# Kernel optimization log

Hardware: AMD Instinct MI355X
Metric: run time of the kernel (lower is better)

The kernel has to match this reference:

```python
import jax, jax.numpy as jnp
import numpy as np

SEQ, BS, D, F, E = 1024, 2, 2048, 2048, 8


def setup_inputs() -> dict:
    key = jax.random.key(0)
    ks = jax.random.split(key, 8)
    s = 0.02  # param init scale
    return {
        "hidden_states": jax.random.normal(ks[0], (SEQ, BS, D), jnp.float32),
        "router_w": jax.random.normal(ks[1], (D, E), jnp.float32) * s,
        "gate_w": jax.random.normal(ks[2], (E, D, F), jnp.float32) * s,
        "up_w": jax.random.normal(ks[3], (E, D, F), jnp.float32) * s,
        "down_w": jax.random.normal(ks[4], (E, F, D), jnp.float32) * s,
        "shared_gate_w": jax.random.normal(ks[5], (D, F), jnp.float32) * s,
        "shared_up_w": jax.random.normal(ks[6], (D, F), jnp.float32) * s,
        "shared_down_w": jax.random.normal(ks[7], (F, D), jnp.float32) * s,
    }


def reference(hidden_states, router_w, gate_w, up_w, down_w,
              shared_gate_w, shared_up_w, shared_down_w):
    S, B, Dm = hidden_states.shape
    x = hidden_states.reshape(-1, Dm)          # [T, D] flattened tokens
    # --- router: top-1 expert, sigmoid gate applied to the selected logit ---
    logits = x @ router_w                      # [T, E]
    expert_idx = jnp.argmax(logits, axis=-1)   # top-1 index, [T]
    score = jax.nn.sigmoid(jnp.max(logits, axis=-1))  # [T]
    xs = x * score[:, None]                    # scale BEFORE expert (Llama4)
    # --- per-expert SwiGLU MLP on masked token sets, scatter-combined ---
    n_experts = router_w.shape[1]
    out = jnp.zeros_like(x)
    for e in range(n_experts):                 # small structural loop over experts
        m = (expert_idx == e)[:, None]
        xe = jnp.where(m, xs, 0.0)             # zeroed dispatch (equiv to gather)
        h = jax.nn.silu(xe @ gate_w[e]) * (xe @ up_w[e])
        out = out + jnp.where(m, h @ down_w[e], 0.0)
    # --- shared expert on all tokens ---
    shared = (jax.nn.silu(x @ shared_gate_w) * (x @ shared_up_w)) @ shared_down_w
    return (out + shared).reshape(S, B, Dm)
```

## Files before the change

### kernel.cpp

```cpp
#include <hip/hip_runtime.h>
#include <stdint.h>
#include <math.h>

#define T_TOK 2048
#define DIM   2048
#define FDIM  2048
#define NE    8

#define BM 128
#define BN 128
#define BK 32
#define LDB 40

typedef unsigned short u16;
typedef short s16x8 __attribute__((ext_vector_type(8)));
typedef float f32x4 __attribute__((ext_vector_type(4)));

__device__ __forceinline__ u16 f2bf(float f) {
    union { float f; unsigned int u; } v; v.f = f;
    unsigned int r = v.u + 0x7FFFu + ((v.u >> 16) & 1u);
    return (u16)(r >> 16);
}

__global__ __launch_bounds__(256) void router_k(
    const float* __restrict__ x, const float* __restrict__ rw,
    float* __restrict__ score, int* __restrict__ eidx, int* __restrict__ counts)
{
    int t = blockIdx.x;
    int tid = threadIdx.x;
    float p[8] = {0.f,0.f,0.f,0.f,0.f,0.f,0.f,0.f};
    const float* xrow = x + (size_t)t * DIM;
    for (int d = tid; d < DIM; d += 256) {
        float xv = xrow[d];
        const float4* r = (const float4*)(rw + (size_t)d * 8);
        float4 r0 = r[0], r1 = r[1];
        p[0] += xv * r0.x; p[1] += xv * r0.y; p[2] += xv * r0.z; p[3] += xv * r0.w;
        p[4] += xv * r1.x; p[5] += xv * r1.y; p[6] += xv * r1.z; p[7] += xv * r1.w;
    }
    #pragma unroll
    for (int off = 32; off > 0; off >>= 1) {
        #pragma unroll
        for (int e = 0; e < 8; ++e) p[e] += __shfl_down(p[e], off);
    }
    __shared__ float red[4][8];
    int wave = tid >> 6, lane = tid & 63;
    if (lane == 0) {
        #pragma unroll
        for (int e = 0; e < 8; ++e) red[wave][e] = p[e];
    }
    __syncthreads();
    if (tid == 0) {
        float lg[8];
        #pragma unroll
        for (int e = 0; e < 8; ++e) lg[e] = red[0][e] + red[1][e] + red[2][e] + red[3][e];
        int best = 0; float bv = lg[0];
        #pragma unroll
        for (int e = 1; e < 8; ++e) { if (lg[e] > bv) { bv = lg[e]; best = e; } }
        score[t] = 1.f / (1.f + expf(-bv));
        eidx[t] = best;
        atomicAdd(&counts[best], 1);
    }
}

__global__ void scan_k(const int* __restrict__ counts, int* __restrict__ offs,
                       int* __restrict__ fill)
{
    if (threadIdx.x == 0 && blockIdx.x == 0) {
        int run = 0;
        for (int e = 0; e < NE; ++e) { offs[e] = run; fill[e] = run; run += counts[e]; }
    }
}

__global__ __launch_bounds__(256) void gather_k(
    const float* __restrict__ x, const float* __restrict__ score,
    const int* __restrict__ eidx, int* __restrict__ fill,
    int* __restrict__ tokmap, u16* __restrict__ xsc, u16* __restrict__ xbf)
{
    int t = blockIdx.x, tid = threadIdx.x;
    __shared__ int sp;
    if (tid == 0) {
        int e = eidx[t];
        int p = atomicAdd(&fill[e], 1);
        tokmap[p] = t;
        sp = p;
    }
    __syncthreads();
    int pos = sp;
    float s = score[t];
    const float4* xr = (const float4*)(x + (size_t)t * DIM);
    float4 a = xr[tid * 2], b = xr[tid * 2 + 1];
    alignas(16) u16 raw[8] = { f2bf(a.x), f2bf(a.y), f2bf(a.z), f2bf(a.w),
                               f2bf(b.x), f2bf(b.y), f2bf(b.z), f2bf(b.w) };
    alignas(16) u16 scl[8] = { f2bf(a.x*s), f2bf(a.y*s), f2bf(a.z*s), f2bf(a.w*s),
                               f2bf(b.x*s), f2bf(b.y*s), f2bf(b.z*s), f2bf(b.w*s) };
    *(s16x8*)(xbf + (size_t)t * DIM + tid * 8)   = *(s16x8*)raw;
    *(s16x8*)(xsc + (size_t)pos * DIM + tid * 8) = *(s16x8*)scl;
}

__device__ __forceinline__ void stageB(const float* __restrict__ W, u16* Bs,
                                       int bn, int bkh)
{
    const float* wp = W + (size_t)bkh * FDIM + bn;
    alignas(16) u16 tmp[16];
    #pragma unroll
    for (int j = 0; j < 16; ++j) tmp[j] = f2bf(wp[(size_t)j * FDIM]);
    *(s16x8*)&Bs[bn * LDB + bkh]     = *(s16x8*)&tmp[0];
    *(s16x8*)&Bs[bn * LDB + bkh + 8] = *(s16x8*)&tmp[8];
}

__global__ __launch_bounds__(256) void gateup_k(
    const u16* __restrict__ xsc, const u16* __restrict__ xbf,
    const float* __restrict__ gate_w, const float* __restrict__ up_w,
    const float* __restrict__ sgw, const float* __restrict__ suw,
    const int* __restrict__ counts, const int* __restrict__ offs,
    u16* __restrict__ Hbf, u16* __restrict__ Hs)
{
    int bid = blockIdx.x;
    int g  = bid >> 8;
    int mt = (bid >> 4) & 15;
    int nt = bid & 15;

    int M; const u16* A; const float* Wg; const float* Wu; u16* Ho;
    if (g < NE) {
        M = counts[g];
        int ro = offs[g];
        A  = xsc + (size_t)ro * DIM;
        Wg = gate_w + (size_t)g * DIM * FDIM;
        Wu = up_w  + (size_t)g * DIM * FDIM;
        Ho = Hbf + (size_t)ro * FDIM;
    } else {
        M = T_TOK; A = xbf; Wg = sgw; Wu = suw; Ho = Hs;
    }
    int m0 = mt * BM;
    if (m0 >= M) return;
    int n0 = nt * BN;

    __shared__ u16 As[BM * BK];
    __shared__ u16 Bg[BN * LDB];
    __shared__ u16 Bu[BN * LDB];

    int tid  = threadIdx.x;
    int lane = tid & 63;
    int wave = tid >> 6;
    int wm = (wave >> 1) * 64;
    int wn = (wave & 1) * 64;

    f32x4 accg[4][4], accu[4][4];
    #pragma unroll
    for (int i = 0; i < 4; ++i)
        #pragma unroll
        for (int j = 0; j < 4; ++j) { accg[i][j] = (f32x4)0.f; accu[i][j] = (f32x4)0.f; }

    int ar = tid >> 2;
    int ac = (tid & 3) * 8;
    int arow0 = min(m0 + ar,      M - 1);
    int arow1 = min(m0 + 64 + ar, M - 1);

    int bn  = tid & 127;
    int bkh = (tid >> 7) * 16;

    int am   = wm + (lane & 15);
    int koff = (lane >> 4) * 8;

    for (int k0 = 0; k0 < DIM; k0 += BK) {
        *(s16x8*)&As[ar * BK + ac]        = *(const s16x8*)&A[(size_t)arow0 * DIM + k0 + ac];
        *(s16x8*)&As[(64 + ar) * BK + ac] = *(const s16x8*)&A[(size_t)arow1 * DIM + k0 + ac];
        stageB(Wg + (size_t)k0 * FDIM + n0, Bg, bn, bkh);
        stageB(Wu + (size_t)k0 * FDIM + n0, Bu, bn, bkh);
        __syncthreads();

        s16x8 af[4];
        #pragma unroll
        for (int i = 0; i < 4; ++i)
            af[i] = *(const s16x8*)&As[(am + i * 16) * BK + koff];
        #pragma unroll
        for (int j = 0; j < 4; ++j) {
            int bc = wn + j * 16 + (lane & 15);
            s16x8 bg = *(const s16x8*)&Bg[bc * LDB + koff];
            s16x8 bu = *(const s16x8*)&Bu[bc * LDB + koff];
            #pragma unroll
            for (int i = 0; i < 4; ++i) {
                accg[i][j] = __builtin_amdgcn_mfma_f32_16x16x32_bf16(af[i], bg, accg[i][j], 0, 0, 0);
                accu[i][j] = __builtin_amdgcn_mfma_f32_16x16x32_bf16(af[i], bu, accu[i][j], 0, 0, 0);
            }
        }
        __syncthreads();
    }

    int rbase = wm + ((lane >> 4) << 2);
    int cbase = n0 + wn + (lane & 15);
    #pragma unroll
    for (int i = 0; i < 4; ++i) {
        #pragma unroll
        for (int j = 0; j < 4; ++j) {
            #pragma unroll
            for (int r = 0; r < 4; ++r) {
                int row = m0 + rbase + i * 16 + r;
                if (row < M) {
                    float gv = accg[i][j][r];
                    float uv = accu[i][j][r];
                    float h = gv / (1.f + expf(-gv)) * uv;
                    Ho[(size_t)row * FDIM + cbase + j * 16] = f2bf(h);
                }
            }
        }
    }
}

__global__ __launch_bounds__(256) void down_k(
    const u16* __restrict__ Hbf, const u16* __restrict__ Hs,
    const float* __restrict__ down_w, const float* __restrict__ sdw,
    const int* __restrict__ counts, const int* __restrict__ offs,
    const int* __restrict__ tokmap, float* __restrict__ out)
{
    int bid = blockIdx.x;
    int g  = bid >> 8;
    int mt = (bid >> 4) & 15;
    int nt = bid & 15;

    int M, ro; const u16* A; const float* W;
    if (g < NE) {
        M = counts[g];
        ro = offs[g];
        A = Hbf + (size_t)ro * FDIM;
        W = down_w + (size_t)g * FDIM * DIM;
    } else {
        M = T_TOK; ro = 0; A = Hs; W = sdw;
    }
    int m0 = mt * BM;
    if (m0 >= M) return;
    int n0 = nt * BN;

    __shared__ u16 As[BM * BK];
    __shared__ u16 Bd[BN * LDB];

    int tid  = threadIdx.x;
    int lane = tid & 63;
    int wave = tid >> 6;
    int wm = (wave >> 1) * 64;
    int wn = (wave & 1) * 64;

    f32x4 acc[4][4];
    #pragma unroll
    for (int i = 0; i < 4; ++i)
        #pragma unroll
        for (int j = 0; j < 4; ++j) acc[i][j] = (f32x4)0.f;

    int ar = tid >> 2;
    int ac = (tid & 3) * 8;
    int arow0 = min(m0 + ar,      M - 1);
    int arow1 = min(m0 + 64 + ar, M - 1);
    int bn  = tid & 127;
    int bkh = (tid >> 7) * 16;

    int am   = wm + (lane & 15);
    int koff = (lane >> 4) * 8;

    for (int k0 = 0; k0 < FDIM; k0 += BK) {
        *(s16x8*)&As[ar * BK + ac]        = *(const s16x8*)&A[(size_t)arow0 * FDIM + k0 + ac];
        *(s16x8*)&As[(64 + ar) * BK + ac] = *(const s16x8*)&A[(size_t)arow1 * FDIM + k0 + ac];
        stageB(W + (size_t)k0 * DIM + n0, Bd, bn, bkh);
        __syncthreads();

        s16x8 af[4];
        #pragma unroll
        for (int i = 0; i < 4; ++i)
            af[i] = *(const s16x8*)&As[(am + i * 16) * BK + koff];
        #pragma unroll
        for (int j = 0; j < 4; ++j) {
            int bc = wn + j * 16 + (lane & 15);
            s16x8 bd = *(const s16x8*)&Bd[bc * LDB + koff];
            #pragma unroll
            for (int i = 0; i < 4; ++i)
                acc[i][j] = __builtin_amdgcn_mfma_f32_16x16x32_bf16(af[i], bd, acc[i][j], 0, 0, 0);
        }
        __syncthreads();
    }

    int rbase = wm + ((lane >> 4) << 2);
    int cbase = n0 + wn + (lane & 15);
    #pragma unroll
    for (int i = 0; i < 4; ++i) {
        #pragma unroll
        for (int r = 0; r < 4; ++r) {
            int row = m0 + rbase + i * 16 + r;
            if (row < M) {
                int tok = (g < NE) ? tokmap[ro + row] : row;
                #pragma unroll
                for (int j = 0; j < 4; ++j)
                    atomicAdd(&out[(size_t)tok * DIM + cbase + j * 16], acc[i][j][r]);
            }
        }
    }
}

extern "C" void kernel_launch(void* const* d_in, const int* in_sizes, int n_in,
                              void* d_out, int out_size, void* d_ws, size_t ws_size,
                              hipStream_t stream) {
    const float* x   = (const float*)d_in[0];
    const float* rw  = (const float*)d_in[1];
    const float* gw  = (const float*)d_in[2];
    const float* uw  = (const float*)d_in[3];
    const float* dw  = (const float*)d_in[4];
    const float* sgw = (const float*)d_in[5];
    const float* suw = (const float*)d_in[6];
    const float* sdw = (const float*)d_in[7];
    float* out = (float*)d_out;

    char* ws = (char*)d_ws;
    float* score = (float*)(ws);
    int* eidx    = (int*)(ws + 8192);
    int* counts  = (int*)(ws + 16384);
    int* fill    = (int*)(ws + 16448);
    int* offs    = (int*)(ws + 16512);
    int* tokmap  = (int*)(ws + 16576);
    u16* xsc = (u16*)(ws + 32768);
    u16* xbf = (u16*)(ws + 32768 + 1ull * 8388608);
    u16* Hbf = (u16*)(ws + 32768 + 2ull * 8388608);
    u16* Hs  = (u16*)(ws + 32768 + 3ull * 8388608);

    hipMemsetAsync(counts, 0, 128, stream);
    hipMemsetAsync(out, 0, (size_t)out_size * sizeof(float), stream);

    router_k<<<T_TOK, 256, 0, stream>>>(x, rw, score, eidx, counts);
    scan_k<<<1, 64, 0, stream>>>(counts, offs, fill);
    gather_k<<<T_TOK, 256, 0, stream>>>(x, score, eidx, fill, tokmap, xsc, xbf);
    gateup_k<<<NE * 256 + 256, 256, 0, stream>>>(xsc, xbf, gw, uw, sgw, suw,
                                                 counts, offs, Hbf, Hs);
    down_k<<<NE * 256 + 256, 256, 0, stream>>>(Hbf, Hs, dw, sdw,
                                               counts, offs, tokmap, out);
}
```

Measured before the change: 792.1 us.

## Pre-transpose weights to bf16 and use direct global-to-LDS loads in GEMMs

Adds a kernel that converts every fp32 weight matrix to bf16 once and transposes it to an N-major layout. The GEMM kernels can then load B tiles with global_load_lds 16-byte transfers instead of strided per-element fp32 loads converted in registers. M tile shrinks to 64, giving more blocks for small expert groups. The shared-expert down pass now writes output directly, which removes the output memset and the atomics; the expert pass then does plain read-add-write, relying on each token hitting one expert. The cost is an extra full pass over all weights (read fp32, write bf16) on every call, plus extra workspace.

```diff
diff --git a/kernel.cpp b/kernel.cpp
--- a/kernel.cpp
+++ b/kernel.cpp
@@ -7,10 +7,10 @@
 #define FDIM  2048
 #define NE    8
 
-#define BM 128
+#define BM 64
 #define BN 128
 #define BK 32
-#define LDB 40
+#define MATSZ 4194304ull
 
 typedef unsigned short u16;
 typedef short s16x8 __attribute__((ext_vector_type(8)));
@@ -20,6 +20,11 @@
     union { float f; unsigned int u; } v; v.f = f;
     unsigned int r = v.u + 0x7FFFu + ((v.u >> 16) & 1u);
     return (u16)(r >> 16);
+}
+
+__device__ __forceinline__ void gload_lds16(const void* g, void* l) {
+    __builtin_amdgcn_global_load_lds((const __attribute__((address_space(1))) void*)g,
+                                     (__attribute__((address_space(3))) void*)l, 16, 0, 0);
 }
 
 __global__ __launch_bounds__(256) void router_k(
@@ -97,100 +102,142 @@
     *(s16x8*)(xsc + (size_t)pos * DIM + tid * 8) = *(s16x8*)scl;
 }
 
-__device__ __forceinline__ void stageB(const float* __restrict__ W, u16* Bs,
-                                       int bn, int bkh)
-{
-    const float* wp = W + (size_t)bkh * FDIM + bn;
-    alignas(16) u16 tmp[16];
-    #pragma unroll
-    for (int j = 0; j < 16; ++j) tmp[j] = f2bf(wp[(size_t)j * FDIM]);
-    *(s16x8*)&Bs[bn * LDB + bkh]     = *(s16x8*)&tmp[0];
-    *(s16x8*)&Bs[bn * LDB + bkh + 8] = *(s16x8*)&tmp[8];
+#define TLDS 260
+__global__ __launch_bounds__(256) void wtrans_k(
+    const float* __restrict__ gw, const float* __restrict__ uw,
+    const float* __restrict__ dwn, const float* __restrict__ sgw,
+    const float* __restrict__ suw, const float* __restrict__ sdw,
+    u16* __restrict__ wt, int mstart)
+{
+    int bid = blockIdx.x;
+    int m = mstart + (bid >> 8);
+    int kt = (bid >> 3) & 31;
+    int nt = bid & 7;
+    const float* src;
+    if      (m < 8)   src = gw  + (size_t)m * MATSZ;
+    else if (m < 16)  src = uw  + (size_t)(m - 8) * MATSZ;
+    else if (m == 16) src = sgw;
+    else if (m == 17) src = suw;
+    else if (m < 26)  src = dwn + (size_t)(m - 18) * MATSZ;
+    else              src = sdw;
+    u16* dst = wt + (size_t)m * MATSZ;
+
+    int k0 = kt * 64, n0 = nt * 256;
+    __shared__ u16 T[64 * TLDS];
+    int t = threadIdx.x;
+    int lw = t >> 6, l = t & 63;
+
+    #pragma unroll 4
+    for (int i = 0; i < 16; ++i) {
+        int kk = lw * 16 + i;
+        float4 v = *(const float4*)&src[(size_t)(k0 + kk) * 2048 + n0 + l * 4];
+        alignas(8) u16 b4[4] = { f2bf(v.x), f2bf(v.y), f2bf(v.z), f2bf(v.w) };
+        *(uint64_t*)&T[kk * TLDS + l * 4] = *(uint64_t*)b4;
+    }
+    __syncthreads();
+
+    int c  = t & 7;
+    int nb = t >> 3;
+    #pragma unroll
+    for (int p = 0; p < 8; ++p) {
+        int n = p * 32 + nb;
+        alignas(16) u16 o[8];
+        #pragma unroll
+        for (int jj = 0; jj < 8; ++jj) {
+            int j = (jj + c) & 7;
+            o[j] = T[(c * 8 + j) * TLDS + n];
+        }
+        *(s16x8*)&dst[(size_t)(n0 + n) * 2048 + k0 + c * 8] = *(s16x8*)o;
+    }
 }
 
 __global__ __launch_bounds__(256) void gateup_k(
     const u16* __restrict__ xsc, const u16* __restrict__ xbf,
-    const float* __restrict__ gate_w, const float* __restrict__ up_w,
-    const float* __restrict__ sgw, const float* __restrict__ suw,
+    const u16* __restrict__ wt,
     const int* __restrict__ counts, const int* __restrict__ offs,
     u16* __restrict__ Hbf, u16* __restrict__ Hs)
 {
     int bid = blockIdx.x;
-    int g  = bid >> 8;
-    int mt = (bid >> 4) & 15;
+    int g  = bid >> 9;
+    int mt = (bid >> 4) & 31;
     int nt = bid & 15;
 
-    int M; const u16* A; const float* Wg; const float* Wu; u16* Ho;
+    int M; const u16* A; const u16* Wg; const u16* Wu; u16* Ho;
     if (g < NE) {
         M = counts[g];
         int ro = offs[g];
         A  = xsc + (size_t)ro * DIM;
-        Wg = gate_w + (size_t)g * DIM * FDIM;
-        Wu = up_w  + (size_t)g * DIM * FDIM;
+        Wg = wt + (size_t)g * MATSZ;
+        Wu = wt + (size_t)(8 + g) * MATSZ;
         Ho = Hbf + (size_t)ro * FDIM;
     } else {
-        M = T_TOK; A = xbf; Wg = sgw; Wu = suw; Ho = Hs;
+        M = T_TOK; A = xbf;
+        Wg = wt + 16 * MATSZ;
+        Wu = wt + 17 * MATSZ;
+        Ho = Hs;
     }
     int m0 = mt * BM;
     if (m0 >= M) return;
     int n0 = nt * BN;
 
-    __shared__ u16 As[BM * BK];
-    __shared__ u16 Bg[BN * LDB];
-    __shared__ u16 Bu[BN * LDB];
-
-    int tid  = threadIdx.x;
-    int lane = tid & 63;
-    int wave = tid >> 6;
-    int wm = (wave >> 1) * 64;
-    int wn = (wave & 1) * 64;
-
-    f32x4 accg[4][4], accu[4][4];
-    #pragma unroll
-    for (int i = 0; i < 4; ++i)
+    __shared__ __align__(128) u16 As[BM * BK];
+    __shared__ __align__(128) u16 Bg[BN * BK];
+    __shared__ __align__(128) u16 Bu[BN * BK];
+
+    int tid = threadIdx.x;
+    int l   = tid & 63;
+    int w   = tid >> 6;
+    int wm = (w >> 1) * 32;
+    int wn = (w & 1) * 64;
+
+    f32x4 accg[2][4], accu[2][4];
+    #pragma unroll
+    for (int i = 0; i < 2; ++i)
         #pragma unroll
         for (int j = 0; j < 4; ++j) { accg[i][j] = (f32x4)0.f; accu[i][j] = (f32x4)0.f; }
 
-    int ar = tid >> 2;
-    int ac = (tid & 3) * 8;
-    int arow0 = min(m0 + ar,      M - 1);
-    int arow1 = min(m0 + 64 + ar, M - 1);
-
-    int bn  = tid & 127;
-    int bkh = (tid >> 7) * 16;
-
-    int am   = wm + (lane & 15);
-    int koff = (lane >> 4) * 8;
+    int rr = l >> 2;
+    int co = (l & 3) * 8;
+    const u16* gA   = A  + (size_t)min(m0 + w * 16 + rr, M - 1) * DIM + co;
+    const u16* gBg0 = Wg + (size_t)(n0 + w * 16 + rr)      * DIM + co;
+    const u16* gBg1 = Wg + (size_t)(n0 + 64 + w * 16 + rr) * DIM + co;
+    const u16* gBu0 = Wu + (size_t)(n0 + w * 16 + rr)      * DIM + co;
+    const u16* gBu1 = Wu + (size_t)(n0 + 64 + w * 16 + rr) * DIM + co;
+    u16* lA   = As + (w * 16) * BK;
+    u16* lBg0 = Bg + (w * 16) * BK;
+    u16* lBg1 = Bg + (64 + w * 16) * BK;
+    u16* lBu0 = Bu + (w * 16) * BK;
+    u16* lBu1 = Bu + (64 + w * 16) * BK;
+
+    int am   = wm + (l & 15);
+    int koff = (l >> 4) * 8;
 
     for (int k0 = 0; k0 < DIM; k0 += BK) {
-        *(s16x8*)&As[ar * BK + ac]        = *(const s16x8*)&A[(size_t)arow0 * DIM + k0 + ac];
-        *(s16x8*)&As[(64 + ar) * BK + ac] = *(const s16x8*)&A[(size_t)arow1 * DIM + k0 + ac];
-        stageB(Wg + (size_t)k0 * FDIM + n0, Bg, bn, bkh);
-        stageB(Wu + (size_t)k0 * FDIM + n0, Bu, bn, bkh);
+        gload_lds16(gA,   lA);
+        gload_lds16(gBg0, lBg0); gload_lds16(gBg1, lBg1);
+        gload_lds16(gBu0, lBu0); gload_lds16(gBu1, lBu1);
+        gA += BK; gBg0 += BK; gBg1 += BK; gBu0 += BK; gBu1 += BK;
         __syncthreads();
 
-        s16x8 af[4];
-        #pragma unroll
-        for (int i = 0; i < 4; ++i)
-            af[i] = *(const s16x8*)&As[(am + i * 16) * BK + koff];
+        s16x8 af0 = *(const s16x8*)&As[am * BK + koff];
+        s16x8 af1 = *(const s16x8*)&As[(am + 16) * BK + koff];
         #pragma unroll
         for (int j = 0; j < 4; ++j) {
-            int bc = wn + j * 16 + (lane & 15);
-            s16x8 bg = *(const s16x8*)&Bg[bc * LDB + koff];
-            s16x8 bu = *(const s16x8*)&Bu[bc * LDB + koff];
-            #pragma unroll
-            for (int i = 0; i < 4; ++i) {
-                accg[i][j] = __builtin_amdgcn_mfma_f32_16x16x32_bf16(af[i], bg, accg[i][j], 0, 0, 0);
-                accu[i][j] = __builtin_amdgcn_mfma_f32_16x16x32_bf16(af[i], bu, accu[i][j], 0, 0, 0);
-            }
+            int bc = wn + j * 16 + (l & 15);
+            s16x8 bg = *(const s16x8*)&Bg[bc * BK + koff];
+            s16x8 bu = *(const s16x8*)&Bu[bc * BK + koff];
+            accg[0][j] = __builtin_amdgcn_mfma_f32_16x16x32_bf16(af0, bg, accg[0][j], 0, 0, 0);
+            accg[1][j] = __builtin_amdgcn_mfma_f32_16x16x32_bf16(af1, bg, accg[1][j], 0, 0, 0);
+            accu[0][j] = __builtin_amdgcn_mfma_f32_16x16x32_bf16(af0, bu, accu[0][j], 0, 0, 0);
+            accu[1][j] = __builtin_amdgcn_mfma_f32_16x16x32_bf16(af1, bu, accu[1][j], 0, 0, 0);
         }
         __syncthreads();
     }
 
-    int rbase = wm + ((lane >> 4) << 2);
-    int cbase = n0 + wn + (lane & 15);
-    #pragma unroll
-    for (int i = 0; i < 4; ++i) {
+    int rbase = wm + ((l >> 4) << 2);
+    int cbase = n0 + wn + (l & 15);
+    #pragma unroll
+    for (int i = 0; i < 2; ++i) {
         #pragma unroll
         for (int j = 0; j < 4; ++j) {
             #pragma unroll
@@ -209,86 +256,88 @@
 
 __global__ __launch_bounds__(256) void down_k(
     const u16* __restrict__ Hbf, const u16* __restrict__ Hs,
-    const float* __restrict__ down_w, const float* __restrict__ sdw,
+    const u16* __restrict__ wt,
     const int* __restrict__ counts, const int* __restrict__ offs,
-    const int* __restrict__ tokmap, float* __restrict__ out)
+    const int* __restrict__ tokmap, float* __restrict__ out, int shared_pass)
 {
     int bid = blockIdx.x;
-    int g  = bid >> 8;
-    int mt = (bid >> 4) & 15;
-    int nt = bid & 15;
-
-    int M, ro; const u16* A; const float* W;
-    if (g < NE) {
-        M = counts[g];
-        ro = offs[g];
+    int g, mt, nt, M, ro; const u16* A; const u16* W;
+    if (shared_pass) {
+        g = NE; mt = bid >> 4; nt = bid & 15;
+        M = T_TOK; ro = 0; A = Hs; W = wt + 26 * MATSZ;
+    } else {
+        g = bid >> 9; mt = (bid >> 4) & 31; nt = bid & 15;
+        M = counts[g]; ro = offs[g];
         A = Hbf + (size_t)ro * FDIM;
-        W = down_w + (size_t)g * FDIM * DIM;
-    } else {
-        M = T_TOK; ro = 0; A = Hs; W = sdw;
+        W = wt + (size_t)(18 + g) * MATSZ;
     }
     int m0 = mt * BM;
     if (m0 >= M) return;
     int n0 = nt * BN;
 
-    __shared__ u16 As[BM * BK];
-    __shared__ u16 Bd[BN * LDB];
-
-    int tid  = threadIdx.x;
-    int lane = tid & 63;
-    int wave = tid >> 6;
-    int wm = (wave >> 1) * 64;
-    int wn = (wave & 1) * 64;
-
-    f32x4 acc[4][4];
-    #pragma unroll
-    for (int i = 0; i < 4; ++i)
+    __shared__ __align__(128) u16 As[BM * BK];
+    __shared__ __align__(128) u16 Bd[BN * BK];
+
+    int tid = threadIdx.x;
+    int l   = tid & 63;
+    int w   = tid >> 6;
+    int wm = (w >> 1) * 32;
+    int wn = (w & 1) * 64;
+
+    f32x4 acc[2][4];
+    #pragma unroll
+    for (int i = 0; i < 2; ++i)
         #pragma unroll
         for (int j = 0; j < 4; ++j) acc[i][j] = (f32x4)0.f;
 
-    int ar = tid >> 2;
-    int ac = (tid & 3) * 8;
-    int arow0 = min(m0 + ar,      M - 1);
-    int arow1 = min(m0 + 64 + ar, M - 1);
-    int bn  = tid & 127;
-    int bkh = (tid >> 7) * 16;
-
-    int am   = wm + (lane & 15);
-    int koff = (lane >> 4) * 8;
+    int rr = l >> 2;
+    int co = (l & 3) * 8;
+    const u16* gA  = A + (size_t)min(m0 + w * 16 + rr, M - 1) * FDIM + co;
+    const u16* gB0 = W + (size_t)(n0 + w * 16 + rr)      * FDIM + co;
+    const u16* gB1 = W + (size_t)(n0 + 64 + w * 16 + rr) * FDIM + co;
+    u16* lA  = As + (w * 16) * BK;
+    u16* lB0 = Bd + (w * 16) * BK;
+    u16* lB1 = Bd + (64 + w * 16) * BK;
+
+    int am   = wm + (l & 15);
+    int koff = (l >> 4) * 8;
 
     for (int k0 = 0; k0 < FDIM; k0 += BK) {
-        *(s16x8*)&As[ar * BK + ac]        = *(const s16x8*)&A[(size_t)arow0 * FDIM + k0 + ac];
-        *(s16x8*)&As[(64 + ar) * BK + ac] = *(const s16x8*)&A[(size_t)arow1 * FDIM + k0 + ac];
-        stageB(W + (size_t)k0 * DIM + n0, Bd, bn, bkh);
+        gload_lds16(gA, lA);
+        gload_lds16(gB0, lB0); gload_lds16(gB1, lB1);
+        gA += BK; gB0 += BK; gB1 += BK;
         __syncthreads();
 
-        s16x8 af[4];
-        #pragma unroll
-        for (int i = 0; i < 4; ++i)
-            af[i] = *(const s16x8*)&As[(am + i * 16) * BK + koff];
+        s16x8 af0 = *(const s16x8*)&As[am * BK + koff];
+        s16x8 af1 = *(const s16x8*)&As[(am + 16) * BK + koff];
         #pragma unroll
         for (int j = 0; j < 4; ++j) {
-            int bc = wn + j * 16 + (lane & 15);
-            s16x8 bd = *(const s16x8*)&Bd[bc * LDB + koff];
-            #pragma unroll
-            for (int i = 0; i < 4; ++i)
-                acc[i][j] = __builtin_amdgcn_mfma_f32_16x16x32_bf16(af[i], bd, acc[i][j], 0, 0, 0);
+            int bc = wn + j * 16 + (l & 15);
+            s16x8 bd = *(const s16x8*)&Bd[bc * BK + koff];
+            acc[0][j] = __builtin_amdgcn_mfma_f32_16x16x32_bf16(af0, bd, acc[0][j], 0, 0, 0);
+            acc[1][j] = __builtin_amdgcn_mfma_f32_16x16x32_bf16(af1, bd, acc[1][j], 0, 0, 0);
         }
         __syncthreads();
     }
 
-    int rbase = wm + ((lane >> 4) << 2);
-    int cbase = n0 + wn + (lane & 15);
-    #pragma unroll
-    for (int i = 0; i < 4; ++i) {
+    int rbase = wm + ((l >> 4) << 2);
+    int cbase = n0 + wn + (l & 15);
+    #pragma unroll
+    for (int i = 0; i < 2; ++i) {
         #pragma unroll
         for (int r = 0; r < 4; ++r) {
             int row = m0 + rbase + i * 16 + r;
             if (row < M) {
-                int tok = (g < NE) ? tokmap[ro + row] : row;
-                #pragma unroll
-                for (int j = 0; j < 4; ++j)
-                    atomicAdd(&out[(size_t)tok * DIM + cbase + j * 16], acc[i][j][r]);
+                if (shared_pass) {
+                    float* dst = out + (size_t)row * DIM;
+                    #pragma unroll
+                    for (int j = 0; j < 4; ++j) dst[cbase + j * 16] = acc[i][j][r];
+                } else {
+                    float* dst = out + (size_t)tokmap[ro + row] * DIM;
+                    #pragma unroll
+                    for (int j = 0; j < 4; ++j)
+                        dst[cbase + j * 16] = dst[cbase + j * 16] + acc[i][j][r];
+                }
             }
         }
     }
@@ -301,7 +350,7 @@
     const float* rw  = (const float*)d_in[1];
     const float* gw  = (const float*)d_in[2];
     const float* uw  = (const float*)d_in[3];
-    const float* dw  = (const float*)d_in[4];
+    const float* dwn = (const float*)d_in[4];
     const float* sgw = (const float*)d_in[5];
     const float* suw = (const float*)d_in[6];
     const float* sdw = (const float*)d_in[7];
@@ -315,18 +364,21 @@
     int* offs    = (int*)(ws + 16512);
     int* tokmap  = (int*)(ws + 16576);
     u16* xsc = (u16*)(ws + 32768);
-    u16* xbf = (u16*)(ws + 32768 + 1ull * 8388608);
-    u16* Hbf = (u16*)(ws + 32768 + 2ull * 8388608);
-    u16* Hs  = (u16*)(ws + 32768 + 3ull * 8388608);
+    u16* xbf = xsc + MATSZ;
+    u16* Hbf = xbf + MATSZ;
+    u16* Hs  = Hbf + MATSZ;
+    u16* wt  = (u16*)(ws + 32768 + 4ull * 8388608 + 16777216);
 
     hipMemsetAsync(counts, 0, 128, stream);
-    hipMemsetAsync(out, 0, (size_t)out_size * sizeof(float), stream);
 
     router_k<<<T_TOK, 256, 0, stream>>>(x, rw, score, eidx, counts);
     scan_k<<<1, 64, 0, stream>>>(counts, offs, fill);
     gather_k<<<T_TOK, 256, 0, stream>>>(x, score, eidx, fill, tokmap, xsc, xbf);
-    gateup_k<<<NE * 256 + 256, 256, 0, stream>>>(xsc, xbf, gw, uw, sgw, suw,
-                                                 counts, offs, Hbf, Hs);
-    down_k<<<NE * 256 + 256, 256, 0, stream>>>(Hbf, Hs, dw, sdw,
-                                               counts, offs, tokmap, out);
-}
+
+    wtrans_k<<<18 * 256, 256, 0, stream>>>(gw, uw, dwn, sgw, suw, sdw, wt, 0);
+    gateup_k<<<9 * 512, 256, 0, stream>>>(xsc, xbf, wt, counts, offs, Hbf, Hs);
+
+    wtrans_k<<<9 * 256, 256, 0, stream>>>(gw, uw, dwn, sgw, suw, sdw, wt, 18);
+    down_k<<<512, 256, 0, stream>>>(Hbf, Hs, wt, counts, offs, tokmap, out, 1);
+    down_k<<<8 * 512, 256, 0, stream>>>(Hbf, Hs, wt, counts, offs, tokmap, out, 0);
+}
```

Measured after the change: 730.4 us. 7.8% less time.
